# Performance work log

Hardware: AMD Instinct MI355X
Metric: run time of the kernel (lower is better)

## Reference

```python
import jax, jax.numpy as jnp
import numpy as np
import math

B, T, E, D = 4, 2048, 1024, 4

def _tau_init(t):
    a = 0.1 ** (1.0 / max(t - 1, 1))
    tt = -math.log(max(a, 1e-10))
    return math.log(math.exp(tt) - 1 + 1e-10)

def causal_ema(b, tau_raw):
    # h_t = alpha * h_{t-1} + b_t with alpha = exp(-softplus(tau_raw));
    # exactly equal to the conv1d with kernel exp(-tau*j) in the original.
    alpha = jnp.exp(-jax.nn.softplus(tau_raw)).astype(b.dtype)
    def step(h, bt):
        h = alpha * h + bt
        return h, h
    h0 = jnp.zeros((b.shape[0], b.shape[2]), b.dtype)
    _, hs = jax.lax.scan(step, h0, jnp.swapaxes(b, 0, 1))  # scan over T
    return jnp.swapaxes(hs, 0, 1)

def setup_inputs():
    key = jax.random.key(0)
    ks = jax.random.split(key, 10)
    s = 0.02
    return {
        "x": jax.random.normal(ks[0], (B, T, E), jnp.float32),
        "tau_ctx": jnp.float32(_tau_init(max(T // 2, 4))),
        "tau_raws": jnp.array([_tau_init(max(T // 2 ** i, 2)) for i in range(D)], jnp.float32),
        "Wg": jax.random.normal(ks[1], (E, 2 * E), jnp.float32) * s,
        "bg": jnp.full((E,), -0.5, jnp.float32),
        "Wn1": jax.random.normal(ks[2], (E // 4, E), jnp.float32) * s,
        "bn1": jnp.zeros((E // 4,), jnp.float32),
        "Wn2": jax.random.normal(ks[3], (D, E // 4), jnp.float32) * s,
        "bn2": jnp.zeros((D,), jnp.float32),
        "blend": jax.random.normal(ks[4], (D, E), jnp.float32) * s,
        "Wsoma": jax.random.normal(ks[5], (E, E), jnp.float32) * s,
        "bsoma": jnp.zeros((E,), jnp.float32),
        "Wtemp": jax.random.normal(ks[6], (E, E), jnp.float32) * s,
        "btemp": jnp.zeros((E,), jnp.float32),
        "Wout": jax.random.normal(ks[7], (E, E), jnp.float32) * s,
        "gamma": jnp.ones((E,), jnp.float32),
        "beta": jnp.zeros((E,), jnp.float32),
    }

def reference(x, tau_ctx, tau_raws, Wg, bg, Wn1, bn1, Wn2, bn2, blend, Wsoma, bsoma, Wtemp, btemp, Wout, gamma, beta):
    ctx = causal_ema(x, tau_ctx)                                   # (B,T,E)
    gate_in = jnp.concatenate([x, ctx], axis=-1)                   # (B,T,2E)
    wg = jax.nn.sigmoid(jnp.einsum('btc,ec->bte', gate_in, Wg) + bg)
    gated = x * wg
    h1 = jax.nn.gelu(jnp.einsum('btc,hc->bth', x, Wn1) + bn1, approximate=False)
    mod = 0.5 + jax.nn.sigmoid(jnp.einsum('bth,dh->btd', h1, Wn2) + bn2)  # (B,T,D)
    # neuromod_ema: modulate input then fixed-alpha EMA, one per dendrite
    traces = jax.vmap(lambda tau, m: causal_ema(gated * m[..., None], tau))(
        tau_raws, jnp.moveaxis(mod, -1, 0))                        # (D,B,T,E)
    blend_w = jax.nn.softmax(blend, axis=0)                        # (D,E)
    temporal = jnp.einsum('dbtc,dc->btc', traces, blend_w)
    gate = jax.nn.sigmoid(jnp.einsum('btc,ec->bte', temporal, Wtemp) + btemp)
    soma = jax.nn.gelu(jnp.einsum('btc,ec->bte', x, Wsoma) + bsoma, approximate=False)
    out = jnp.einsum('btc,ec->bte', soma * gate, Wout)
    mu = out.mean(-1, keepdims=True)
    var = out.var(-1, keepdims=True)
    return (out - mu) / jnp.sqrt(var + 1e-5) * gamma + beta
```

## Files before the change

### kernel.cpp

```cpp
#include <hip/hip_runtime.h>
#include <math.h>

#define B_DIM 4
#define T_DIM 2048
#define E_DIM 1024
#define M_ROWS (B_DIM*T_DIM)
#define NC 32
#define CL (T_DIM/NC)

typedef short short8 __attribute__((ext_vector_type(8)));
typedef float f32x4 __attribute__((ext_vector_type(4)));

__device__ __forceinline__ float bf2f(unsigned short u){
  union { unsigned int i; float f; } c; c.i = ((unsigned int)u) << 16; return c.f;
}
__device__ __forceinline__ unsigned short f2bf(float f){
  union { float f; unsigned int i; } c; c.f = f;
  unsigned int u = c.i;
  return (unsigned short)((u + 0x7FFFu + ((u >> 16) & 1u)) >> 16);
}
__device__ __forceinline__ unsigned int pack2(float a, float b){
  return (unsigned int)f2bf(a) | ((unsigned int)f2bf(b) << 16);
}
__device__ __forceinline__ float sigf(float x){ return 1.f/(1.f+__expf(-x)); }
__device__ __forceinline__ float geluf(float x){ return 0.5f*x*(1.f+erff(x*0.70710678118f)); }

__device__ __forceinline__ void glds16(const unsigned short* g, unsigned short* l){
  __builtin_amdgcn_global_load_lds((const __attribute__((address_space(1))) void*)g,
                                   (__attribute__((address_space(3))) void*)l, 16, 0, 0);
}

__device__ __forceinline__ void cvt4(const float* __restrict__ s, unsigned short* __restrict__ d){
  float4 v = *(const float4*)s;
  uint2 p; p.x = pack2(v.x, v.y); p.y = pack2(v.z, v.w);
  *(uint2*)d = p;
}

__global__ __launch_bounds__(256) void conv_all_k(
    const float* __restrict__ Wg, const float* __restrict__ Wsoma,
    const float* __restrict__ Wn1, const float* __restrict__ Wtemp,
    const float* __restrict__ Wout, const float* __restrict__ bsoma,
    const float* __restrict__ bn1,
    unsigned short* __restrict__ wg_bf, unsigned short* __restrict__ wsn1,
    unsigned short* __restrict__ wtemp_bf, unsigned short* __restrict__ wout_bf,
    float* __restrict__ bsn1){
  int u = blockIdx.x*256 + threadIdx.x;
  if (u < 524288){ cvt4(Wg + (size_t)u*4, wg_bf + (size_t)u*4); }
  else if (u < 786432){ u -= 524288; cvt4(Wsoma + (size_t)u*4, wsn1 + (size_t)u*4); }
  else if (u < 851968){ u -= 786432; cvt4(Wn1 + (size_t)u*4, wsn1 + 1048576 + (size_t)u*4); }
  else if (u < 1114112){ u -= 851968; cvt4(Wtemp + (size_t)u*4, wtemp_bf + (size_t)u*4); }
  else if (u < 1376256){ u -= 1114112; cvt4(Wout + (size_t)u*4, wout_bf + (size_t)u*4); }
  else if (u < 1376576){
    u -= 1376256; int i = u*4;
    float4 v = (i < 1024) ? *(const float4*)&bsoma[i] : *(const float4*)&bn1[i-1024];
    *(float4*)&bsn1[i] = v;
  }
}

__global__ __launch_bounds__(256) void ctx_carry_k(const float* __restrict__ x,
                                                   const float* __restrict__ tau_ctx,
                                                   float* __restrict__ car){
  int gid = blockIdx.x*256 + threadIdx.x;
  int e2 = (gid & 511)*2, bc = gid >> 9;
  int b = bc >> 5, chunk = bc & 31;
  float alpha = 1.f/(1.f+expf(tau_ctx[0]));
  const float2* xp = (const float2*)(x + ((size_t)b*T_DIM + chunk*CL)*E_DIM + e2);
  float h0 = 0.f, h1 = 0.f;
  #pragma unroll 8
  for (int t = 0; t < CL; t++){
    float2 v = xp[(size_t)t*512];
    h0 = alpha*h0 + v.x; h1 = alpha*h1 + v.y;
  }
  *(float2*)&car[(size_t)bc*E_DIM + e2] = make_float2(h0, h1);
}

__global__ __launch_bounds__(256) void ctx_scan_k(const float* __restrict__ x,
                                                  const float* __restrict__ tau_ctx,
                                                  const float* __restrict__ car,
                                                  unsigned short* __restrict__ gatein){
  int gid = blockIdx.x*256 + threadIdx.x;
  int e2 = (gid & 511)*2, bc = gid >> 9;
  int b = bc >> 5, chunk = bc & 31;
  float alpha = 1.f/(1.f+expf(tau_ctx[0]));
  float alphaL = powf(alpha, (float)CL);
  float h0 = 0.f, h1 = 0.f;
  for (int j = 0; j < chunk; j++){
    float2 c = *(const float2*)&car[(size_t)(b*NC + j)*E_DIM + e2];
    h0 = alphaL*h0 + c.x; h1 = alphaL*h1 + c.y;
  }
  const float2* xp = (const float2*)(x + ((size_t)b*T_DIM + chunk*CL)*E_DIM + e2);
  unsigned int* op = (unsigned int*)(gatein + ((size_t)(b*T_DIM + chunk*CL))*2048 + e2);
  #pragma unroll 4
  for (int t = 0; t < CL; t++){
    float2 v = xp[(size_t)t*512];
    h0 = alpha*h0 + v.x; h1 = alpha*h1 + v.y;
    op[(size_t)t*1024]       = pack2(v.x, v.y);
    op[(size_t)t*1024 + 512] = pack2(h0, h1);
  }
}

__global__ __launch_bounds__(256) void dend_carry_k(const unsigned short* __restrict__ gated,
                                                    const float* __restrict__ mod,
                                                    const float* __restrict__ tau_raws,
                                                    float* __restrict__ car){
  int gid = blockIdx.x*256 + threadIdx.x;
  int e2 = (gid & 511)*2, bc = gid >> 9;
  int b = bc >> 5, chunk = bc & 31;
  float a[4];
  #pragma unroll
  for (int d = 0; d < 4; d++) a[d] = 1.f/(1.f+expf(tau_raws[d]));
  const ushort2* gp = (const ushort2*)(gated + ((size_t)(b*T_DIM + chunk*CL))*E_DIM + e2);
  const float4* mp = (const float4*)(mod + (size_t)(b*T_DIM + chunk*CL)*4);
  float hx[4] = {0,0,0,0}, hy[4] = {0,0,0,0};
  #pragma unroll 4
  for (int t = 0; t < CL; t++){
    ushort2 gv = gp[(size_t)t*512];
    float gx = bf2f(gv.x), gy = bf2f(gv.y);
    float4 m4 = mp[t];
    hx[0] = a[0]*hx[0] + gx*m4.x; hy[0] = a[0]*hy[0] + gy*m4.x;
    hx[1] = a[1]*hx[1] + gx*m4.y; hy[1] = a[1]*hy[1] + gy*m4.y;
    hx[2] = a[2]*hx[2] + gx*m4.z; hy[2] = a[2]*hy[2] + gy*m4.z;
    hx[3] = a[3]*hx[3] + gx*m4.w; hy[3] = a[3]*hy[3] + gy*m4.w;
  }
  #pragma unroll
  for (int d = 0; d < 4; d++)
    *(float2*)&car[(size_t)d*131072 + (size_t)bc*E_DIM + e2] = make_float2(hx[d], hy[d]);
}

__global__ __launch_bounds__(256) void dend_scan_k(const unsigned short* __restrict__ gated,
                                                   const float* __restrict__ mod,
                                                   const float* __restrict__ tau_raws,
                                                   const float* __restrict__ car,
                                                   const float* __restrict__ blend,
                                                   unsigned short* __restrict__ temporal){
  int gid = blockIdx.x*256 + threadIdx.x;
  int e2 = (gid & 511)*2, bc = gid >> 9;
  int b = bc >> 5, chunk = bc & 31;
  float a[4], hx[4], hy[4];
  #pragma unroll
  for (int d = 0; d < 4; d++) a[d] = 1.f/(1.f+expf(tau_raws[d]));
  #pragma unroll
  for (int d = 0; d < 4; d++){
    float aL = powf(a[d], (float)CL);
    float h0 = 0.f, h1 = 0.f;
    for (int j = 0; j < chunk; j++){
      float2 c = *(const float2*)&car[(size_t)d*131072 + (size_t)(b*NC + j)*E_DIM + e2];
      h0 = aL*h0 + c.x; h1 = aL*h1 + c.y;
    }
    hx[d] = h0; hy[d] = h1;
  }
  float blx[4], bly[4];
  #pragma unroll
  for (int d = 0; d < 4; d++){
    float2 bl = *(const float2*)&blend[(size_t)d*E_DIM + e2];
    blx[d] = bl.x; bly[d] = bl.y;
  }
  float mxx = fmaxf(fmaxf(blx[0],blx[1]), fmaxf(blx[2],blx[3]));
  float mxy = fmaxf(fmaxf(bly[0],bly[1]), fmaxf(bly[2],bly[3]));
  float wx[4], wy[4], sx = 0.f, sy = 0.f;
  #pragma unroll
  for (int d = 0; d < 4; d++){ wx[d] = __expf(blx[d]-mxx); sx += wx[d];
                               wy[d] = __expf(bly[d]-mxy); sy += wy[d]; }
  float ix = 1.f/sx, iy = 1.f/sy;
  #pragma unroll
  for (int d = 0; d < 4; d++){ wx[d] *= ix; wy[d] *= iy; }

  const ushort2* gp = (const ushort2*)(gated + ((size_t)(b*T_DIM + chunk*CL))*E_DIM + e2);
  const float4* mp = (const float4*)(mod + (size_t)(b*T_DIM + chunk*CL)*4);
  unsigned int* op = (unsigned int*)(temporal + ((size_t)(b*T_DIM + chunk*CL))*E_DIM + e2);
  #pragma unroll 4
  for (int t = 0; t < CL; t++){
    ushort2 gv = gp[(size_t)t*512];
    float gx = bf2f(gv.x), gy = bf2f(gv.y);
    float4 m4 = mp[t];
    hx[0] = a[0]*hx[0] + gx*m4.x; hy[0] = a[0]*hy[0] + gy*m4.x;
    hx[1] = a[1]*hx[1] + gx*m4.y; hy[1] = a[1]*hy[1] + gy*m4.y;
    hx[2] = a[2]*hx[2] + gx*m4.z; hy[2] = a[2]*hy[2] + gy*m4.z;
    hx[3] = a[3]*hx[3] + gx*m4.w; hy[3] = a[3]*hy[3] + gy*m4.w;
    float tvx = wx[0]*hx[0] + wx[1]*hx[1] + wx[2]*hx[2] + wx[3]*hx[3];
    float tvy = wy[0]*hy[0] + wy[1]*hy[1] + wy[2]*hy[2] + wy[3]*hy[3];
    op[(size_t)t*512] = pack2(tvx, tvy);
  }
}

__global__ __launch_bounds__(256) void mod_k(const unsigned short* __restrict__ h1,
                                             const float* __restrict__ Wn2,
                                             const float* __restrict__ bn2,
                                             float* __restrict__ mod){
  int wave = threadIdx.x >> 6, lane = threadIdx.x & 63;
  int m = blockIdx.x*4 + wave;
  float p0=0.f,p1=0.f,p2=0.f,p3=0.f;
  for (int c = lane; c < 256; c += 64){
    float h = bf2f(h1[(size_t)m*256 + c]);
    p0 += h*Wn2[0*256 + c]; p1 += h*Wn2[1*256 + c];
    p2 += h*Wn2[2*256 + c]; p3 += h*Wn2[3*256 + c];
  }
  #pragma unroll
  for (int off = 32; off > 0; off >>= 1){
    p0 += __shfl_down(p0, off); p1 += __shfl_down(p1, off);
    p2 += __shfl_down(p2, off); p3 += __shfl_down(p3, off);
  }
  if (lane == 0){
    mod[(size_t)m*4 + 0] = 0.5f + sigf(p0 + bn2[0]);
    mod[(size_t)m*4 + 1] = 0.5f + sigf(p1 + bn2[1]);
    mod[(size_t)m*4 + 2] = 0.5f + sigf(p2 + bn2[2]);
    mod[(size_t)m*4 + 3] = 0.5f + sigf(p3 + bn2[3]);
  }
}

__global__ __launch_bounds__(256, 2) void gemm1_k(
    const unsigned short* __restrict__ gatein,
    const unsigned short* __restrict__ wg_bf,
    const unsigned short* __restrict__ wsn1,
    const float* __restrict__ bg,
    const float* __restrict__ bsn1,
    unsigned short* __restrict__ gated,
    unsigned short* __restrict__ soma,
    unsigned short* __restrict__ h1)
{
  __shared__ unsigned short sA[2][4096];
  __shared__ unsigned short sB[2][4096];
  const int tid = threadIdx.x;
  const int wv = tid >> 6, lane = tid & 63;
  const int quad = lane >> 4, l15 = lane & 15;
  const int wm = (wv & 1) * 64, wn = (wv >> 1) * 64;
  const int row0 = blockIdx.x * 128;
  const int by = blockIdx.y;

  int mode, colw0, K;
  const unsigned short* Bw;
  const float* bias;
  if (by < 8)       { mode = 0; colw0 = by*128;            Bw = wg_bf + (size_t)colw0*2048; K = 2048; bias = bg   + colw0; }
  else if (by < 16) { mode = 1; colw0 = (by-8)*128;        Bw = wsn1  + (size_t)colw0*1024; K = 1024; bias = bsn1 + colw0; }
  else              { mode = 2; colw0 = 1024 + (by-16)*128; Bw = wsn1 + (size_t)colw0*1024; K = 1024; bias = bsn1 + colw0; }

  const int r = tid >> 2, kc = (tid & 3) * 8;
  const unsigned short* pa0 = gatein + (size_t)(row0 + r)*2048      + kc;
  const unsigned short* pa1 = gatein + (size_t)(row0 + 64 + r)*2048 + kc;
  const unsigned short* pb0 = Bw + (size_t)r*K        + kc;
  const unsigned short* pb1 = Bw + (size_t)(64 + r)*K + kc;

  f32x4 acc[4][4];
  #pragma unroll
  for (int i = 0; i < 4; i++)
    #pragma unroll
    for (int j = 0; j < 4; j++) acc[i][j] = (f32x4){0.f,0.f,0.f,0.f};

  glds16(pa0, &sA[0][wv*512]);
  glds16(pa1, &sA[0][2048 + wv*512]);
  glds16(pb0, &sB[0][wv*512]);
  glds16(pb1, &sB[0][2048 + wv*512]);

  const int nk = K >> 5;
  for (int it = 0; it < nk; it++){
    __syncthreads();
    const int cur = it & 1, nxt = cur ^ 1;
    if (it + 1 < nk){
      const int ko = (it + 1) << 5;
      glds16(pa0 + ko, &sA[nxt][wv*512]);
      glds16(pa1 + ko, &sA[nxt][2048 + wv*512]);
      glds16(pb0 + ko, &sB[nxt][wv*512]);
      glds16(pb1 + ko, &sB[nxt][2048 + wv*512]);
    }
    short8 afr[4], bfr[4];
    #pragma unroll
    for (int i = 0; i < 4; i++) afr[i] = *(const short8*)&sA[cur][(wm + i*16 + l15)*32 + quad*8];
    #pragma unroll
    for (int j = 0; j < 4; j++) bfr[j] = *(const short8*)&sB[cur][(wn + j*16 + l15)*32 + quad*8];
    #pragma unroll
    for (int i = 0; i < 4; i++)
      #pragma unroll
      for (int j = 0; j < 4; j++)
        acc[i][j] = __builtin_amdgcn_mfma_f32_16x16x32_bf16(afr[i], bfr[j], acc[i][j], 0, 0, 0);
  }

  if (mode == 0){
    #pragma unroll
    for (int i = 0; i < 4; i++)
      #pragma unroll
      for (int j = 0; j < 4; j++){
        const int lc = wn + j*16 + l15;
        const int col = colw0 + lc;
        #pragma unroll
        for (int rr = 0; rr < 4; rr++){
          const int row = row0 + wm + i*16 + quad*4 + rr;
          float v = acc[i][j][rr] + bias[lc];
          float xv = bf2f(gatein[(size_t)row*2048 + col]);
          gated[(size_t)row*1024 + col] = f2bf(xv * sigf(v));
        }
      }
  } else if (mode == 1){
    #pragma unroll
    for (int i = 0; i < 4; i++)
      #pragma unroll
      for (int j = 0; j < 4; j++){
        const int lc = wn + j*16 + l15;
        const int col = colw0 + lc;
        #pragma unroll
        for (int rr = 0; rr < 4; rr++){
          const int row = row0 + wm + i*16 + quad*4 + rr;
          float v = acc[i][j][rr] + bias[lc];
          soma[(size_t)row*1024 + col] = f2bf(geluf(v));
        }
      }
  } else {
    #pragma unroll
    for (int i = 0; i < 4; i++)
      #pragma unroll
      for (int j = 0; j < 4; j++){
        const int lc = wn + j*16 + l15;
        const int col = colw0 - 1024 + lc;
        #pragma unroll
        for (int rr = 0; rr < 4; rr++){
          const int row = row0 + wm + i*16 + quad*4 + rr;
          float v = acc[i][j][rr] + bias[lc];
          h1[(size_t)row*256 + col] = f2bf(geluf(v));
        }
      }
  }
}

template<int EPI>
__global__ __launch_bounds__(256, 2) void gemm_k(
    const unsigned short* __restrict__ A,
    const unsigned short* __restrict__ Bw,
    const float* __restrict__ bias,
    const unsigned short* __restrict__ ebf,
    void* __restrict__ outp)
{
  __shared__ unsigned short sA[2][4096];
  __shared__ unsigned short sB[2][4096];
  const int tid = threadIdx.x;
  const int wv = tid >> 6, lane = tid & 63;
  const int quad = lane >> 4, l15 = lane & 15;
  const int wm = (wv & 1) * 64, wn = (wv >> 1) * 64;
  const int row0 = blockIdx.x * 128, col0 = blockIdx.y * 128;

  const int r = tid >> 2, kc = (tid & 3) * 8;
  const unsigned short* pa0 = A  + (size_t)(row0 + r)*1024      + kc;
  const unsigned short* pa1 = A  + (size_t)(row0 + 64 + r)*1024 + kc;
  const unsigned short* pb0 = Bw + (size_t)(col0 + r)*1024      + kc;
  const unsigned short* pb1 = Bw + (size_t)(col0 + 64 + r)*1024 + kc;

  f32x4 acc[4][4];
  #pragma unroll
  for (int i = 0; i < 4; i++)
    #pragma unroll
    for (int j = 0; j < 4; j++) acc[i][j] = (f32x4){0.f,0.f,0.f,0.f};

  glds16(pa0, &sA[0][wv*512]);
  glds16(pa1, &sA[0][2048 + wv*512]);
  glds16(pb0, &sB[0][wv*512]);
  glds16(pb1, &sB[0][2048 + wv*512]);

  for (int it = 0; it < 32; it++){
    __syncthreads();
    const int cur = it & 1, nxt = cur ^ 1;
    if (it + 1 < 32){
      const int ko = (it + 1) << 5;
      glds16(pa0 + ko, &sA[nxt][wv*512]);
      glds16(pa1 + ko, &sA[nxt][2048 + wv*512]);
      glds16(pb0 + ko, &sB[nxt][wv*512]);
      glds16(pb1 + ko, &sB[nxt][2048 + wv*512]);
    }
    short8 afr[4], bfr[4];
    #pragma unroll
    for (int i = 0; i < 4; i++) afr[i] = *(const short8*)&sA[cur][(wm + i*16 + l15)*32 + quad*8];
    #pragma unroll
    for (int j = 0; j < 4; j++) bfr[j] = *(const short8*)&sB[cur][(wn + j*16 + l15)*32 + quad*8];
    #pragma unroll
    for (int i = 0; i < 4; i++)
      #pragma unroll
      for (int j = 0; j < 4; j++)
        acc[i][j] = __builtin_amdgcn_mfma_f32_16x16x32_bf16(afr[i], bfr[j], acc[i][j], 0, 0, 0);
  }

  #pragma unroll
  for (int i = 0; i < 4; i++)
    #pragma unroll
    for (int j = 0; j < 4; j++){
      const int col = col0 + wn + j*16 + l15;
      #pragma unroll
      for (int rr = 0; rr < 4; rr++){
        const int row = row0 + wm + i*16 + quad*4 + rr;
        float v = acc[i][j][rr];
        size_t o = (size_t)row*1024 + col;
        if (EPI == 2){
          v += bias[col];
          ((unsigned short*)outp)[o] = f2bf(sigf(v) * bf2f(ebf[o]));
        } else {
          ((float*)outp)[o] = v;
        }
      }
    }
}

__global__ __launch_bounds__(256) void ln_k(const float* __restrict__ in,
                                            const float* __restrict__ gamma,
                                            const float* __restrict__ beta,
                                            float* __restrict__ out){
  __shared__ float s1[4], s2[4];
  int row = blockIdx.x, tid = threadIdx.x;
  float4 v = *(const float4*)&in[(size_t)row*1024 + tid*4];
  float s = v.x+v.y+v.z+v.w;
  float q = v.x*v.x+v.y*v.y+v.z*v.z+v.w*v.w;
  #pragma unroll
  for (int off = 32; off > 0; off >>= 1){ s += __shfl_down(s, off); q += __shfl_down(q, off); }
  int wave = tid >> 6, lane = tid & 63;
  if (lane == 0){ s1[wave] = s; s2[wave] = q; }
  __syncthreads();
  s = s1[0]+s1[1]+s1[2]+s1[3];
  q = s2[0]+s2[1]+s2[2]+s2[3];
  float mu = s*(1.f/1024.f);
  float var = q*(1.f/1024.f) - mu*mu;
  float rs = rsqrtf(var + 1e-5f);
  int c = tid*4;
  float4 g = *(const float4*)&gamma[c];
  float4 bb = *(const float4*)&beta[c];
  float4 o;
  o.x = (v.x-mu)*rs*g.x + bb.x;
  o.y = (v.y-mu)*rs*g.y + bb.y;
  o.z = (v.z-mu)*rs*g.z + bb.z;
  o.w = (v.w-mu)*rs*g.w + bb.w;
  *(float4*)&out[(size_t)row*1024 + c] = o;
}

extern "C" void kernel_launch(void* const* d_in, const int* in_sizes, int n_in,
                              void* d_out, int out_size, void* d_ws, size_t ws_size,
                              hipStream_t stream) {
  const float* x        = (const float*)d_in[0];
  const float* tau_ctx  = (const float*)d_in[1];
  const float* tau_raws = (const float*)d_in[2];
  const float* Wg       = (const float*)d_in[3];
  const float* bg       = (const float*)d_in[4];
  const float* Wn1      = (const float*)d_in[5];
  const float* bn1      = (const float*)d_in[6];
  const float* Wn2      = (const float*)d_in[7];
  const float* bn2      = (const float*)d_in[8];
  const float* blend    = (const float*)d_in[9];
  const float* Wsoma    = (const float*)d_in[10];
  const float* bsoma    = (const float*)d_in[11];
  const float* Wtemp    = (const float*)d_in[12];
  const float* btemp    = (const float*)d_in[13];
  const float* Wout     = (const float*)d_in[14];
  const float* gamma    = (const float*)d_in[15];
  const float* beta     = (const float*)d_in[16];

  char* ws = (char*)d_ws;
  unsigned short* gatein   = (unsigned short*)(ws + 0);
  float*          out_pre  = (float*)(ws + 0);
  unsigned short* wg_bf    = (unsigned short*)(ws + 33554432);
  unsigned short* wsn1     = (unsigned short*)(ws + 37748736);
  unsigned short* wtemp_bf = (unsigned short*)(ws + 40370176);
  unsigned short* wout_bf  = (unsigned short*)(ws + 42467328);
  float*          bsn1     = (float*)(ws + 44564480);
  unsigned short* h1_bf    = (unsigned short*)(ws + 44572672);
  float*          car_d    = (float*)(ws + 44572672);
  float*          car_ctx  = (float*)(ws + 48766976);
  float*          modbuf   = (float*)(ws + 48766976);
  unsigned short* gated    = (unsigned short*)(ws + 49291264);
  unsigned short* sg       = gated;
  unsigned short* temporal = (unsigned short*)(ws + 66068480);
  unsigned short* soma     = (unsigned short*)(ws + 82845696);

  conv_all_k<<<dim3(5378), dim3(256), 0, stream>>>(Wg, Wsoma, Wn1, Wtemp, Wout, bsoma, bn1,
                                                   wg_bf, wsn1, wtemp_bf, wout_bf, bsn1);

  ctx_carry_k<<<dim3(256), dim3(256), 0, stream>>>(x, tau_ctx, car_ctx);
  ctx_scan_k <<<dim3(256), dim3(256), 0, stream>>>(x, tau_ctx, car_ctx, gatein);

  gemm1_k<<<dim3(64, 18), dim3(256), 0, stream>>>(gatein, wg_bf, wsn1, bg, bsn1,
                                                  gated, soma, h1_bf);

  mod_k<<<dim3(M_ROWS/4), dim3(256), 0, stream>>>(h1_bf, Wn2, bn2, modbuf);

  dend_carry_k<<<dim3(256), dim3(256), 0, stream>>>(gated, modbuf, tau_raws, car_d);
  dend_scan_k <<<dim3(256), dim3(256), 0, stream>>>(gated, modbuf, tau_raws, car_d, blend, temporal);

  gemm_k<2><<<dim3(64, 8), dim3(256), 0, stream>>>(temporal, wtemp_bf, btemp, soma, sg);

  gemm_k<3><<<dim3(64, 8), dim3(256), 0, stream>>>(sg, wout_bf, nullptr, nullptr, out_pre);

  ln_k<<<dim3(M_ROWS), dim3(256), 0, stream>>>(out_pre, gamma, beta, (float*)d_out);
}
```

Baseline: 342.8 us.

## Fuse weight conversion with ctx carry, shrink GEMM tiles, one-wave-per-row LayerNorm

The weight-conversion kernel and the ctx carry kernel are merged into a single launch. The K=2048 gate GEMM in gemm1 is split into 64-row tiles, giving 26 column groups instead of 18. gemm_k now uses 64x128 tiles, doubling its grid. LayerNorm handles one row per wave with xor shuffles, which removes the LDS reduction and the block barrier. The aim is better CU occupancy and load balance on the 256-CU GPU and less launch overhead, at the cost of more B-tile reloads per output.

After: 358.1 us. 4.5% more time.

```diff
diff --git a/kernel.cpp b/kernel.cpp
--- a/kernel.cpp
+++ b/kernel.cpp
@@ -36,42 +36,42 @@
   *(uint2*)d = p;
 }
 
-__global__ __launch_bounds__(256) void conv_all_k(
+__global__ __launch_bounds__(256) void conv_carry_k(
     const float* __restrict__ Wg, const float* __restrict__ Wsoma,
     const float* __restrict__ Wn1, const float* __restrict__ Wtemp,
     const float* __restrict__ Wout, const float* __restrict__ bsoma,
     const float* __restrict__ bn1,
     unsigned short* __restrict__ wg_bf, unsigned short* __restrict__ wsn1,
     unsigned short* __restrict__ wtemp_bf, unsigned short* __restrict__ wout_bf,
-    float* __restrict__ bsn1){
-  int u = blockIdx.x*256 + threadIdx.x;
-  if (u < 524288){ cvt4(Wg + (size_t)u*4, wg_bf + (size_t)u*4); }
-  else if (u < 786432){ u -= 524288; cvt4(Wsoma + (size_t)u*4, wsn1 + (size_t)u*4); }
-  else if (u < 851968){ u -= 786432; cvt4(Wn1 + (size_t)u*4, wsn1 + 1048576 + (size_t)u*4); }
-  else if (u < 1114112){ u -= 851968; cvt4(Wtemp + (size_t)u*4, wtemp_bf + (size_t)u*4); }
-  else if (u < 1376256){ u -= 1114112; cvt4(Wout + (size_t)u*4, wout_bf + (size_t)u*4); }
-  else if (u < 1376576){
-    u -= 1376256; int i = u*4;
-    float4 v = (i < 1024) ? *(const float4*)&bsoma[i] : *(const float4*)&bn1[i-1024];
-    *(float4*)&bsn1[i] = v;
-  }
-}
-
-__global__ __launch_bounds__(256) void ctx_carry_k(const float* __restrict__ x,
-                                                   const float* __restrict__ tau_ctx,
-                                                   float* __restrict__ car){
-  int gid = blockIdx.x*256 + threadIdx.x;
-  int e2 = (gid & 511)*2, bc = gid >> 9;
-  int b = bc >> 5, chunk = bc & 31;
-  float alpha = 1.f/(1.f+expf(tau_ctx[0]));
-  const float2* xp = (const float2*)(x + ((size_t)b*T_DIM + chunk*CL)*E_DIM + e2);
-  float h0 = 0.f, h1 = 0.f;
-  #pragma unroll 8
-  for (int t = 0; t < CL; t++){
-    float2 v = xp[(size_t)t*512];
-    h0 = alpha*h0 + v.x; h1 = alpha*h1 + v.y;
-  }
-  *(float2*)&car[(size_t)bc*E_DIM + e2] = make_float2(h0, h1);
+    float* __restrict__ bsn1,
+    const float* __restrict__ x, const float* __restrict__ tau_ctx,
+    float* __restrict__ car){
+  if (blockIdx.x < 5378){
+    int u = blockIdx.x*256 + threadIdx.x;
+    if (u < 524288){ cvt4(Wg + (size_t)u*4, wg_bf + (size_t)u*4); }
+    else if (u < 786432){ u -= 524288; cvt4(Wsoma + (size_t)u*4, wsn1 + (size_t)u*4); }
+    else if (u < 851968){ u -= 786432; cvt4(Wn1 + (size_t)u*4, wsn1 + 1048576 + (size_t)u*4); }
+    else if (u < 1114112){ u -= 851968; cvt4(Wtemp + (size_t)u*4, wtemp_bf + (size_t)u*4); }
+    else if (u < 1376256){ u -= 1114112; cvt4(Wout + (size_t)u*4, wout_bf + (size_t)u*4); }
+    else if (u < 1376576){
+      u -= 1376256; int i = u*4;
+      float4 v = (i < 1024) ? *(const float4*)&bsoma[i] : *(const float4*)&bn1[i-1024];
+      *(float4*)&bsn1[i] = v;
+    }
+  } else {
+    int gid = (blockIdx.x - 5378)*256 + threadIdx.x;
+    int e2 = (gid & 511)*2, bc = gid >> 9;
+    int b = bc >> 5, chunk = bc & 31;
+    float alpha = 1.f/(1.f+expf(tau_ctx[0]));
+    const float2* xp = (const float2*)(x + ((size_t)b*T_DIM + chunk*CL)*E_DIM + e2);
+    float h0 = 0.f, h1 = 0.f;
+    #pragma unroll 8
+    for (int t = 0; t < CL; t++){
+      float2 v = xp[(size_t)t*512];
+      h0 = alpha*h0 + v.x; h1 = alpha*h1 + v.y;
+    }
+    *(float2*)&car[(size_t)bc*E_DIM + e2] = make_float2(h0, h1);
+  }
 }
 
 __global__ __launch_bounds__(256) void ctx_scan_k(const float* __restrict__ x,
@@ -223,60 +223,51 @@
   const int tid = threadIdx.x;
   const int wv = tid >> 6, lane = tid & 63;
   const int quad = lane >> 4, l15 = lane & 15;
-  const int wm = (wv & 1) * 64, wn = (wv >> 1) * 64;
-  const int row0 = blockIdx.x * 128;
   const int by = blockIdx.y;
-
-  int mode, colw0, K;
-  const unsigned short* Bw;
-  const float* bias;
-  if (by < 8)       { mode = 0; colw0 = by*128;            Bw = wg_bf + (size_t)colw0*2048; K = 2048; bias = bg   + colw0; }
-  else if (by < 16) { mode = 1; colw0 = (by-8)*128;        Bw = wsn1  + (size_t)colw0*1024; K = 1024; bias = bsn1 + colw0; }
-  else              { mode = 2; colw0 = 1024 + (by-16)*128; Bw = wsn1 + (size_t)colw0*1024; K = 1024; bias = bsn1 + colw0; }
-
   const int r = tid >> 2, kc = (tid & 3) * 8;
-  const unsigned short* pa0 = gatein + (size_t)(row0 + r)*2048      + kc;
-  const unsigned short* pa1 = gatein + (size_t)(row0 + 64 + r)*2048 + kc;
-  const unsigned short* pb0 = Bw + (size_t)r*K        + kc;
-  const unsigned short* pb1 = Bw + (size_t)(64 + r)*K + kc;
-
-  f32x4 acc[4][4];
-  #pragma unroll
-  for (int i = 0; i < 4; i++)
-    #pragma unroll
-    for (int j = 0; j < 4; j++) acc[i][j] = (f32x4){0.f,0.f,0.f,0.f};
-
-  glds16(pa0, &sA[0][wv*512]);
-  glds16(pa1, &sA[0][2048 + wv*512]);
-  glds16(pb0, &sB[0][wv*512]);
-  glds16(pb1, &sB[0][2048 + wv*512]);
-
-  const int nk = K >> 5;
-  for (int it = 0; it < nk; it++){
-    __syncthreads();
-    const int cur = it & 1, nxt = cur ^ 1;
-    if (it + 1 < nk){
-      const int ko = (it + 1) << 5;
-      glds16(pa0 + ko, &sA[nxt][wv*512]);
-      glds16(pa1 + ko, &sA[nxt][2048 + wv*512]);
-      glds16(pb0 + ko, &sB[nxt][wv*512]);
-      glds16(pb1 + ko, &sB[nxt][2048 + wv*512]);
-    }
-    short8 afr[4], bfr[4];
-    #pragma unroll
-    for (int i = 0; i < 4; i++) afr[i] = *(const short8*)&sA[cur][(wm + i*16 + l15)*32 + quad*8];
-    #pragma unroll
-    for (int j = 0; j < 4; j++) bfr[j] = *(const short8*)&sB[cur][(wn + j*16 + l15)*32 + quad*8];
-    #pragma unroll
-    for (int i = 0; i < 4; i++)
-      #pragma unroll
-      for (int j = 0; j < 4; j++)
-        acc[i][j] = __builtin_amdgcn_mfma_f32_16x16x32_bf16(afr[i], bfr[j], acc[i][j], 0, 0, 0);
-  }
-
-  if (mode == 0){
-    #pragma unroll
-    for (int i = 0; i < 4; i++)
+
+  if (by < 16){
+    const int colw0 = (by & 7) * 128;
+    const int row0 = blockIdx.x * 128 + ((by >> 3) ? 64 : 0);
+    const unsigned short* Bw = wg_bf + (size_t)colw0 * 2048;
+    const unsigned short* pa0 = gatein + (size_t)(row0 + r)*2048 + kc;
+    const unsigned short* pb0 = Bw + (size_t)r*2048        + kc;
+    const unsigned short* pb1 = Bw + (size_t)(64 + r)*2048 + kc;
+    const int wm = (wv & 1) * 32, wn = (wv >> 1) * 64;
+
+    f32x4 acc[2][4];
+    #pragma unroll
+    for (int i = 0; i < 2; i++)
+      #pragma unroll
+      for (int j = 0; j < 4; j++) acc[i][j] = (f32x4){0.f,0.f,0.f,0.f};
+
+    glds16(pa0, &sA[0][wv*512]);
+    glds16(pb0, &sB[0][wv*512]);
+    glds16(pb1, &sB[0][2048 + wv*512]);
+
+    for (int it = 0; it < 64; it++){
+      __syncthreads();
+      const int cur = it & 1, nxt = cur ^ 1;
+      if (it + 1 < 64){
+        const int ko = (it + 1) << 5;
+        glds16(pa0 + ko, &sA[nxt][wv*512]);
+        glds16(pb0 + ko, &sB[nxt][wv*512]);
+        glds16(pb1 + ko, &sB[nxt][2048 + wv*512]);
+      }
+      short8 afr[2], bfr[4];
+      #pragma unroll
+      for (int i = 0; i < 2; i++) afr[i] = *(const short8*)&sA[cur][(wm + i*16 + l15)*32 + quad*8];
+      #pragma unroll
+      for (int j = 0; j < 4; j++) bfr[j] = *(const short8*)&sB[cur][(wn + j*16 + l15)*32 + quad*8];
+      #pragma unroll
+      for (int i = 0; i < 2; i++)
+        #pragma unroll
+        for (int j = 0; j < 4; j++)
+          acc[i][j] = __builtin_amdgcn_mfma_f32_16x16x32_bf16(afr[i], bfr[j], acc[i][j], 0, 0, 0);
+    }
+
+    #pragma unroll
+    for (int i = 0; i < 2; i++)
       #pragma unroll
       for (int j = 0; j < 4; j++){
         const int lc = wn + j*16 + l15;
@@ -284,37 +275,68 @@
         #pragma unroll
         for (int rr = 0; rr < 4; rr++){
           const int row = row0 + wm + i*16 + quad*4 + rr;
-          float v = acc[i][j][rr] + bias[lc];
+          float v = acc[i][j][rr] + bg[col];
           float xv = bf2f(gatein[(size_t)row*2048 + col]);
           gated[(size_t)row*1024 + col] = f2bf(xv * sigf(v));
         }
       }
-  } else if (mode == 1){
+  } else {
+    const int ish1 = (by >= 24);
+    const int colw0 = ish1 ? (by - 24)*128 : (by - 16)*128;
+    const int row0 = blockIdx.x * 128;
+    const unsigned short* Bw = wsn1 + (size_t)(ish1 ? 1024 + colw0 : colw0) * 1024;
+    const float* bias = bsn1 + (ish1 ? 1024 + colw0 : colw0);
+    const unsigned short* pa0 = gatein + (size_t)(row0 + r)*2048      + kc;
+    const unsigned short* pa1 = gatein + (size_t)(row0 + 64 + r)*2048 + kc;
+    const unsigned short* pb0 = Bw + (size_t)r*1024        + kc;
+    const unsigned short* pb1 = Bw + (size_t)(64 + r)*1024 + kc;
+    const int wm = (wv & 1) * 64, wn = (wv >> 1) * 64;
+
+    f32x4 acc[4][4];
+    #pragma unroll
+    for (int i = 0; i < 4; i++)
+      #pragma unroll
+      for (int j = 0; j < 4; j++) acc[i][j] = (f32x4){0.f,0.f,0.f,0.f};
+
+    glds16(pa0, &sA[0][wv*512]);
+    glds16(pa1, &sA[0][2048 + wv*512]);
+    glds16(pb0, &sB[0][wv*512]);
+    glds16(pb1, &sB[0][2048 + wv*512]);
+
+    for (int it = 0; it < 32; it++){
+      __syncthreads();
+      const int cur = it & 1, nxt = cur ^ 1;
+      if (it + 1 < 32){
+        const int ko = (it + 1) << 5;
+        glds16(pa0 + ko, &sA[nxt][wv*512]);
+        glds16(pa1 + ko, &sA[nxt][2048 + wv*512]);
+        glds16(pb0 + ko, &sB[nxt][wv*512]);
+        glds16(pb1 + ko, &sB[nxt][2048 + wv*512]);
+      }
+      short8 afr[4], bfr[4];
+      #pragma unroll
+      for (int i = 0; i < 4; i++) afr[i] = *(const short8*)&sA[cur][(wm + i*16 + l15)*32 + quad*8];
+      #pragma unroll
+      for (int j = 0; j < 4; j++) bfr[j] = *(const short8*)&sB[cur][(wn + j*16 + l15)*32 + quad*8];
+      #pragma unroll
+      for (int i = 0; i < 4; i++)
+        #pragma unroll
+        for (int j = 0; j < 4; j++)
+          acc[i][j] = __builtin_amdgcn_mfma_f32_16x16x32_bf16(afr[i], bfr[j], acc[i][j], 0, 0, 0);
+    }
+
     #pragma unroll
     for (int i = 0; i < 4; i++)
       #pragma unroll
       for (int j = 0; j < 4; j++){
         const int lc = wn + j*16 + l15;
-        const int col = colw0 + lc;
         #pragma unroll
         for (int rr = 0; rr < 4; rr++){
           const int row = row0 + wm + i*16 + quad*4 + rr;
           float v = acc[i][j][rr] + bias[lc];
-          soma[(size_t)row*1024 + col] = f2bf(geluf(v));
-        }
-      }
-  } else {
-    #pragma unroll
-    for (int i = 0; i < 4; i++)
-      #pragma unroll
-      for (int j = 0; j < 4; j++){
-        const int lc = wn + j*16 + l15;
-        const int col = colw0 - 1024 + lc;
-        #pragma unroll
-        for (int rr = 0; rr < 4; rr++){
-          const int row = row0 + wm + i*16 + quad*4 + rr;
-          float v = acc[i][j][rr] + bias[lc];
-          h1[(size_t)row*256 + col] = f2bf(geluf(v));
+          float g = geluf(v);
+          if (ish1) h1[(size_t)row*256 + colw0 + lc] = f2bf(g);
+          else      soma[(size_t)row*1024 + colw0 + lc] = f2bf(g);
         }
       }
   }
@@ -328,28 +350,26 @@
     const unsigned short* __restrict__ ebf,
     void* __restrict__ outp)
 {
-  __shared__ unsigned short sA[2][4096];
+  __shared__ unsigned short sA[2][2048];
   __shared__ unsigned short sB[2][4096];
   const int tid = threadIdx.x;
   const int wv = tid >> 6, lane = tid & 63;
   const int quad = lane >> 4, l15 = lane & 15;
-  const int wm = (wv & 1) * 64, wn = (wv >> 1) * 64;
-  const int row0 = blockIdx.x * 128, col0 = blockIdx.y * 128;
+  const int wm = (wv & 1) * 32, wn = (wv >> 1) * 64;
+  const int row0 = blockIdx.x * 64, col0 = blockIdx.y * 128;
 
   const int r = tid >> 2, kc = (tid & 3) * 8;
   const unsigned short* pa0 = A  + (size_t)(row0 + r)*1024      + kc;
-  const unsigned short* pa1 = A  + (size_t)(row0 + 64 + r)*1024 + kc;
   const unsigned short* pb0 = Bw + (size_t)(col0 + r)*1024      + kc;
   const unsigned short* pb1 = Bw + (size_t)(col0 + 64 + r)*1024 + kc;
 
-  f32x4 acc[4][4];
-  #pragma unroll
-  for (int i = 0; i < 4; i++)
+  f32x4 acc[2][4];
+  #pragma unroll
+  for (int i = 0; i < 2; i++)
     #pragma unroll
     for (int j = 0; j < 4; j++) acc[i][j] = (f32x4){0.f,0.f,0.f,0.f};
 
   glds16(pa0, &sA[0][wv*512]);
-  glds16(pa1, &sA[0][2048 + wv*512]);
   glds16(pb0, &sB[0][wv*512]);
   glds16(pb1, &sB[0][2048 + wv*512]);
 
@@ -359,24 +379,23 @@
     if (it + 1 < 32){
       const int ko = (it + 1) << 5;
       glds16(pa0 + ko, &sA[nxt][wv*512]);
-      glds16(pa1 + ko, &sA[nxt][2048 + wv*512]);
       glds16(pb0 + ko, &sB[nxt][wv*512]);
       glds16(pb1 + ko, &sB[nxt][2048 + wv*512]);
     }
-    short8 afr[4], bfr[4];
-    #pragma unroll
-    for (int i = 0; i < 4; i++) afr[i] = *(const short8*)&sA[cur][(wm + i*16 + l15)*32 + quad*8];
+    short8 afr[2], bfr[4];
+    #pragma unroll
+    for (int i = 0; i < 2; i++) afr[i] = *(const short8*)&sA[cur][(wm + i*16 + l15)*32 + quad*8];
     #pragma unroll
     for (int j = 0; j < 4; j++) bfr[j] = *(const short8*)&sB[cur][(wn + j*16 + l15)*32 + quad*8];
     #pragma unroll
-    for (int i = 0; i < 4; i++)
+    for (int i = 0; i < 2; i++)
       #pragma unroll
       for (int j = 0; j < 4; j++)
         acc[i][j] = __builtin_amdgcn_mfma_f32_16x16x32_bf16(afr[i], bfr[j], acc[i][j], 0, 0, 0);
   }
 
   #pragma unroll
-  for (int i = 0; i < 4; i++)
+  for (int i = 0; i < 2; i++)
     #pragma unroll
     for (int j = 0; j < 4; j++){
       const int col = col0 + wn + j*16 + l15;
@@ -399,30 +418,38 @@
                                             const float* __restrict__ gamma,
                                             const float* __restrict__ beta,
                                             float* __restrict__ out){
-  __shared__ float s1[4], s2[4];
-  int row = blockIdx.x, tid = threadIdx.x;
-  float4 v = *(const float4*)&in[(size_t)row*1024 + tid*4];
-  float s = v.x+v.y+v.z+v.w;
-  float q = v.x*v.x+v.y*v.y+v.z*v.z+v.w*v.w;
-  #pragma unroll
-  for (int off = 32; off > 0; off >>= 1){ s += __shfl_down(s, off); q += __shfl_down(q, off); }
-  int wave = tid >> 6, lane = tid & 63;
-  if (lane == 0){ s1[wave] = s; s2[wave] = q; }
-  __syncthreads();
-  s = s1[0]+s1[1]+s1[2]+s1[3];
-  q = s2[0]+s2[1]+s2[2]+s2[3];
+  int wv = threadIdx.x >> 6, lane = threadIdx.x & 63;
+  int row = blockIdx.x*4 + wv;
+  const float4* ip = (const float4*)&in[(size_t)row*1024];
+  float4 v[4];
+  float s = 0.f, q = 0.f;
+  #pragma unroll
+  for (int k = 0; k < 4; k++){
+    v[k] = ip[lane + 64*k];
+    s += v[k].x + v[k].y + v[k].z + v[k].w;
+    q += v[k].x*v[k].x + v[k].y*v[k].y + v[k].z*v[k].z + v[k].w*v[k].w;
+  }
+  #pragma unroll
+  for (int off = 32; off > 0; off >>= 1){
+    s += __shfl_xor(s, off); q += __shfl_xor(q, off);
+  }
   float mu = s*(1.f/1024.f);
   float var = q*(1.f/1024.f) - mu*mu;
   float rs = rsqrtf(var + 1e-5f);
-  int c = tid*4;
-  float4 g = *(const float4*)&gamma[c];
-  float4 bb = *(const float4*)&beta[c];
-  float4 o;
-  o.x = (v.x-mu)*rs*g.x + bb.x;
-  o.y = (v.y-mu)*rs*g.y + bb.y;
-  o.z = (v.z-mu)*rs*g.z + bb.z;
-  o.w = (v.w-mu)*rs*g.w + bb.w;
-  *(float4*)&out[(size_t)row*1024 + c] = o;
+  const float4* gp = (const float4*)gamma;
+  const float4* bp = (const float4*)beta;
+  float4* op = (float4*)&out[(size_t)row*1024];
+  #pragma unroll
+  for (int k = 0; k < 4; k++){
+    int idx = lane + 64*k;
+    float4 g = gp[idx], bb = bp[idx];
+    float4 o;
+    o.x = (v[k].x-mu)*rs*g.x + bb.x;
+    o.y = (v[k].y-mu)*rs*g.y + bb.y;
+    o.z = (v[k].z-mu)*rs*g.z + bb.z;
+    o.w = (v[k].w-mu)*rs*g.w + bb.w;
+    op[idx] = o;
+  }
 }
 
 extern "C" void kernel_launch(void* const* d_in, const int* in_sizes, int n_in,
@@ -463,13 +490,13 @@
   unsigned short* temporal = (unsigned short*)(ws + 66068480);
   unsigned short* soma     = (unsigned short*)(ws + 82845696);
 
-  conv_all_k<<<dim3(5378), dim3(256), 0, stream>>>(Wg, Wsoma, Wn1, Wtemp, Wout, bsoma, bn1,
-                                                   wg_bf, wsn1, wtemp_bf, wout_bf, bsn1);
-
-  ctx_carry_k<<<dim3(256), dim3(256), 0, stream>>>(x, tau_ctx, car_ctx);
-  ctx_scan_k <<<dim3(256), dim3(256), 0, stream>>>(x, tau_ctx, car_ctx, gatein);
-
-  gemm1_k<<<dim3(64, 18), dim3(256), 0, stream>>>(gatein, wg_bf, wsn1, bg, bsn1,
+  conv_carry_k<<<dim3(5634), dim3(256), 0, stream>>>(Wg, Wsoma, Wn1, Wtemp, Wout, bsoma, bn1,
+                                                     wg_bf, wsn1, wtemp_bf, wout_bf, bsn1,
+                                                     x, tau_ctx, car_ctx);
+
+  ctx_scan_k<<<dim3(256), dim3(256), 0, stream>>>(x, tau_ctx, car_ctx, gatein);
+
+  gemm1_k<<<dim3(64, 26), dim3(256), 0, stream>>>(gatein, wg_bf, wsn1, bg, bsn1,
                                                   gated, soma, h1_bf);
 
   mod_k<<<dim3(M_ROWS/4), dim3(256), 0, stream>>>(h1_bf, Wn2, bn2, modbuf);
@@ -477,9 +504,9 @@
   dend_carry_k<<<dim3(256), dim3(256), 0, stream>>>(gated, modbuf, tau_raws, car_d);
   dend_scan_k <<<dim3(256), dim3(256), 0, stream>>>(gated, modbuf, tau_raws, car_d, blend, temporal);
 
-  gemm_k<2><<<dim3(64, 8), dim3(256), 0, stream>>>(temporal, wtemp_bf, btemp, soma, sg);
-
-  gemm_k<3><<<dim3(64, 8), dim3(256), 0, stream>>>(sg, wout_bf, nullptr, nullptr, out_pre);
-
-  ln_k<<<dim3(M_ROWS), dim3(256), 0, stream>>>(out_pre, gamma, beta, (float*)d_out);
-}
+  gemm_k<2><<<dim3(128, 8), dim3(256), 0, stream>>>(temporal, wtemp_bf, btemp, soma, sg);
+
+  gemm_k<3><<<dim3(128, 8), dim3(256), 0, stream>>>(sg, wout_bf, nullptr, nullptr, out_pre);
+
+  ln_k<<<dim3(M_ROWS/4), dim3(256), 0, stream>>>(out_pre, gamma, beta, (float*)d_out);
+}
```

## Fuse weight conversion with ctx carry, relayout GEMM LDS tiles, per-wave layernorm

Applied to the files above, without the earlier changes.

Merges the weight-conversion kernel and the context-carry kernel into one launch, dispatching on block index, to save a launch and let the two independent jobs overlap. Both GEMM kernels change their global-to-LDS load mapping so that each wave loads one k-slice of 8 elements for 64 rows. The LDS tile becomes k-group-major, which changes the fragment read addresses and is meant to reduce bank conflicts. Layernorm now uses one wave per row with shuffle-xor reductions and no shared memory or block barrier.

Measured after the change: 421.8 us. 23.0% more time.

```diff
diff --git a/kernel.cpp b/kernel.cpp
--- a/kernel.cpp
+++ b/kernel.cpp
@@ -36,42 +36,42 @@
   *(uint2*)d = p;
 }
 
-__global__ __launch_bounds__(256) void conv_all_k(
+__global__ __launch_bounds__(256) void conv_carry_k(
     const float* __restrict__ Wg, const float* __restrict__ Wsoma,
     const float* __restrict__ Wn1, const float* __restrict__ Wtemp,
     const float* __restrict__ Wout, const float* __restrict__ bsoma,
     const float* __restrict__ bn1,
     unsigned short* __restrict__ wg_bf, unsigned short* __restrict__ wsn1,
     unsigned short* __restrict__ wtemp_bf, unsigned short* __restrict__ wout_bf,
-    float* __restrict__ bsn1){
-  int u = blockIdx.x*256 + threadIdx.x;
-  if (u < 524288){ cvt4(Wg + (size_t)u*4, wg_bf + (size_t)u*4); }
-  else if (u < 786432){ u -= 524288; cvt4(Wsoma + (size_t)u*4, wsn1 + (size_t)u*4); }
-  else if (u < 851968){ u -= 786432; cvt4(Wn1 + (size_t)u*4, wsn1 + 1048576 + (size_t)u*4); }
-  else if (u < 1114112){ u -= 851968; cvt4(Wtemp + (size_t)u*4, wtemp_bf + (size_t)u*4); }
-  else if (u < 1376256){ u -= 1114112; cvt4(Wout + (size_t)u*4, wout_bf + (size_t)u*4); }
-  else if (u < 1376576){
-    u -= 1376256; int i = u*4;
-    float4 v = (i < 1024) ? *(const float4*)&bsoma[i] : *(const float4*)&bn1[i-1024];
-    *(float4*)&bsn1[i] = v;
-  }
-}
-
-__global__ __launch_bounds__(256) void ctx_carry_k(const float* __restrict__ x,
-                                                   const float* __restrict__ tau_ctx,
-                                                   float* __restrict__ car){
-  int gid = blockIdx.x*256 + threadIdx.x;
-  int e2 = (gid & 511)*2, bc = gid >> 9;
-  int b = bc >> 5, chunk = bc & 31;
-  float alpha = 1.f/(1.f+expf(tau_ctx[0]));
-  const float2* xp = (const float2*)(x + ((size_t)b*T_DIM + chunk*CL)*E_DIM + e2);
-  float h0 = 0.f, h1 = 0.f;
-  #pragma unroll 8
-  for (int t = 0; t < CL; t++){
-    float2 v = xp[(size_t)t*512];
-    h0 = alpha*h0 + v.x; h1 = alpha*h1 + v.y;
-  }
-  *(float2*)&car[(size_t)bc*E_DIM + e2] = make_float2(h0, h1);
+    float* __restrict__ bsn1,
+    const float* __restrict__ x, const float* __restrict__ tau_ctx,
+    float* __restrict__ car){
+  if (blockIdx.x < 5378){
+    int u = blockIdx.x*256 + threadIdx.x;
+    if (u < 524288){ cvt4(Wg + (size_t)u*4, wg_bf + (size_t)u*4); }
+    else if (u < 786432){ u -= 524288; cvt4(Wsoma + (size_t)u*4, wsn1 + (size_t)u*4); }
+    else if (u < 851968){ u -= 786432; cvt4(Wn1 + (size_t)u*4, wsn1 + 1048576 + (size_t)u*4); }
+    else if (u < 1114112){ u -= 851968; cvt4(Wtemp + (size_t)u*4, wtemp_bf + (size_t)u*4); }
+    else if (u < 1376256){ u -= 1114112; cvt4(Wout + (size_t)u*4, wout_bf + (size_t)u*4); }
+    else if (u < 1376576){
+      u -= 1376256; int i = u*4;
+      float4 v = (i < 1024) ? *(const float4*)&bsoma[i] : *(const float4*)&bn1[i-1024];
+      *(float4*)&bsn1[i] = v;
+    }
+  } else {
+    int gid = (blockIdx.x - 5378)*256 + threadIdx.x;
+    int e2 = (gid & 511)*2, bc = gid >> 9;
+    int b = bc >> 5, chunk = bc & 31;
+    float alpha = 1.f/(1.f+expf(tau_ctx[0]));
+    const float2* xp = (const float2*)(x + ((size_t)b*T_DIM + chunk*CL)*E_DIM + e2);
+    float h0 = 0.f, h1 = 0.f;
+    #pragma unroll 8
+    for (int t = 0; t < CL; t++){
+      float2 v = xp[(size_t)t*512];
+      h0 = alpha*h0 + v.x; h1 = alpha*h1 + v.y;
+    }
+    *(float2*)&car[(size_t)bc*E_DIM + e2] = make_float2(h0, h1);
+  }
 }
 
 __global__ __launch_bounds__(256) void ctx_scan_k(const float* __restrict__ x,
@@ -230,15 +230,14 @@
   int mode, colw0, K;
   const unsigned short* Bw;
   const float* bias;
-  if (by < 8)       { mode = 0; colw0 = by*128;            Bw = wg_bf + (size_t)colw0*2048; K = 2048; bias = bg   + colw0; }
-  else if (by < 16) { mode = 1; colw0 = (by-8)*128;        Bw = wsn1  + (size_t)colw0*1024; K = 1024; bias = bsn1 + colw0; }
-  else              { mode = 2; colw0 = 1024 + (by-16)*128; Bw = wsn1 + (size_t)colw0*1024; K = 1024; bias = bsn1 + colw0; }
-
-  const int r = tid >> 2, kc = (tid & 3) * 8;
-  const unsigned short* pa0 = gatein + (size_t)(row0 + r)*2048      + kc;
-  const unsigned short* pa1 = gatein + (size_t)(row0 + 64 + r)*2048 + kc;
-  const unsigned short* pb0 = Bw + (size_t)r*K        + kc;
-  const unsigned short* pb1 = Bw + (size_t)(64 + r)*K + kc;
+  if (by < 8)       { mode = 0; colw0 = by*128;             Bw = wg_bf + (size_t)colw0*2048; K = 2048; bias = bg   + colw0; }
+  else if (by < 16) { mode = 1; colw0 = (by-8)*128;         Bw = wsn1  + (size_t)colw0*1024; K = 1024; bias = bsn1 + colw0; }
+  else              { mode = 2; colw0 = 1024 + (by-16)*128; Bw = wsn1  + (size_t)colw0*1024; K = 1024; bias = bsn1 + colw0; }
+
+  const unsigned short* pa0 = gatein + (size_t)(row0 + lane)*2048 + wv*8;
+  const unsigned short* pa1 = pa0 + (size_t)64*2048;
+  const unsigned short* pb0 = Bw + (size_t)lane*K + wv*8;
+  const unsigned short* pb1 = pb0 + (size_t)64*K;
 
   f32x4 acc[4][4];
   #pragma unroll
@@ -246,10 +245,10 @@
     #pragma unroll
     for (int j = 0; j < 4; j++) acc[i][j] = (f32x4){0.f,0.f,0.f,0.f};
 
-  glds16(pa0, &sA[0][wv*512]);
-  glds16(pa1, &sA[0][2048 + wv*512]);
-  glds16(pb0, &sB[0][wv*512]);
-  glds16(pb1, &sB[0][2048 + wv*512]);
+  glds16(pa0, &sA[0][wv*1024]);
+  glds16(pa1, &sA[0][wv*1024 + 512]);
+  glds16(pb0, &sB[0][wv*1024]);
+  glds16(pb1, &sB[0][wv*1024 + 512]);
 
   const int nk = K >> 5;
   for (int it = 0; it < nk; it++){
@@ -257,16 +256,16 @@
     const int cur = it & 1, nxt = cur ^ 1;
     if (it + 1 < nk){
       const int ko = (it + 1) << 5;
-      glds16(pa0 + ko, &sA[nxt][wv*512]);
-      glds16(pa1 + ko, &sA[nxt][2048 + wv*512]);
-      glds16(pb0 + ko, &sB[nxt][wv*512]);
-      glds16(pb1 + ko, &sB[nxt][2048 + wv*512]);
+      glds16(pa0 + ko, &sA[nxt][wv*1024]);
+      glds16(pa1 + ko, &sA[nxt][wv*1024 + 512]);
+      glds16(pb0 + ko, &sB[nxt][wv*1024]);
+      glds16(pb1 + ko, &sB[nxt][wv*1024 + 512]);
     }
     short8 afr[4], bfr[4];
     #pragma unroll
-    for (int i = 0; i < 4; i++) afr[i] = *(const short8*)&sA[cur][(wm + i*16 + l15)*32 + quad*8];
-    #pragma unroll
-    for (int j = 0; j < 4; j++) bfr[j] = *(const short8*)&sB[cur][(wn + j*16 + l15)*32 + quad*8];
+    for (int i = 0; i < 4; i++) afr[i] = *(const short8*)&sA[cur][(quad*128 + wm + i*16 + l15)*8];
+    #pragma unroll
+    for (int j = 0; j < 4; j++) bfr[j] = *(const short8*)&sB[cur][(quad*128 + wn + j*16 + l15)*8];
     #pragma unroll
     for (int i = 0; i < 4; i++)
       #pragma unroll
@@ -336,11 +335,10 @@
   const int wm = (wv & 1) * 64, wn = (wv >> 1) * 64;
   const int row0 = blockIdx.x * 128, col0 = blockIdx.y * 128;
 
-  const int r = tid >> 2, kc = (tid & 3) * 8;
-  const unsigned short* pa0 = A  + (size_t)(row0 + r)*1024      + kc;
-  const unsigned short* pa1 = A  + (size_t)(row0 + 64 + r)*1024 + kc;
-  const unsigned short* pb0 = Bw + (size_t)(col0 + r)*1024      + kc;
-  const unsigned short* pb1 = Bw + (size_t)(col0 + 64 + r)*1024 + kc;
+  const unsigned short* pa0 = A  + (size_t)(row0 + lane)*1024 + wv*8;
+  const unsigned short* pa1 = pa0 + (size_t)64*1024;
+  const unsigned short* pb0 = Bw + (size_t)(col0 + lane)*1024 + wv*8;
+  const unsigned short* pb1 = pb0 + (size_t)64*1024;
 
   f32x4 acc[4][4];
   #pragma unroll
@@ -348,26 +346,26 @@
     #pragma unroll
     for (int j = 0; j < 4; j++) acc[i][j] = (f32x4){0.f,0.f,0.f,0.f};
 
-  glds16(pa0, &sA[0][wv*512]);
-  glds16(pa1, &sA[0][2048 + wv*512]);
-  glds16(pb0, &sB[0][wv*512]);
-  glds16(pb1, &sB[0][2048 + wv*512]);
+  glds16(pa0, &sA[0][wv*1024]);
+  glds16(pa1, &sA[0][wv*1024 + 512]);
+  glds16(pb0, &sB[0][wv*1024]);
+  glds16(pb1, &sB[0][wv*1024 + 512]);
 
   for (int it = 0; it < 32; it++){
     __syncthreads();
     const int cur = it & 1, nxt = cur ^ 1;
     if (it + 1 < 32){
       const int ko = (it + 1) << 5;
-      glds16(pa0 + ko, &sA[nxt][wv*512]);
-      glds16(pa1 + ko, &sA[nxt][2048 + wv*512]);
-      glds16(pb0 + ko, &sB[nxt][wv*512]);
-      glds16(pb1 + ko, &sB[nxt][2048 + wv*512]);
+      glds16(pa0 + ko, &sA[nxt][wv*1024]);
+      glds16(pa1 + ko, &sA[nxt][wv*1024 + 512]);
+      glds16(pb0 + ko, &sB[nxt][wv*1024]);
+      glds16(pb1 + ko, &sB[nxt][wv*1024 + 512]);
     }
     short8 afr[4], bfr[4];
     #pragma unroll
-    for (int i = 0; i < 4; i++) afr[i] = *(const short8*)&sA[cur][(wm + i*16 + l15)*32 + quad*8];
-    #pragma unroll
-    for (int j = 0; j < 4; j++) bfr[j] = *(const short8*)&sB[cur][(wn + j*16 + l15)*32 + quad*8];
+    for (int i = 0; i < 4; i++) afr[i] = *(const short8*)&sA[cur][(quad*128 + wm + i*16 + l15)*8];
+    #pragma unroll
+    for (int j = 0; j < 4; j++) bfr[j] = *(const short8*)&sB[cur][(quad*128 + wn + j*16 + l15)*8];
     #pragma unroll
     for (int i = 0; i < 4; i++)
       #pragma unroll
@@ -399,30 +397,38 @@
                                             const float* __restrict__ gamma,
                                             const float* __restrict__ beta,
                                             float* __restrict__ out){
-  __shared__ float s1[4], s2[4];
-  int row = blockIdx.x, tid = threadIdx.x;
-  float4 v = *(const float4*)&in[(size_t)row*1024 + tid*4];
-  float s = v.x+v.y+v.z+v.w;
-  float q = v.x*v.x+v.y*v.y+v.z*v.z+v.w*v.w;
-  #pragma unroll
-  for (int off = 32; off > 0; off >>= 1){ s += __shfl_down(s, off); q += __shfl_down(q, off); }
-  int wave = tid >> 6, lane = tid & 63;
-  if (lane == 0){ s1[wave] = s; s2[wave] = q; }
-  __syncthreads();
-  s = s1[0]+s1[1]+s1[2]+s1[3];
-  q = s2[0]+s2[1]+s2[2]+s2[3];
+  int wv = threadIdx.x >> 6, lane = threadIdx.x & 63;
+  int row = blockIdx.x*4 + wv;
+  const float4* ip = (const float4*)&in[(size_t)row*1024];
+  float4 v[4];
+  float s = 0.f, q = 0.f;
+  #pragma unroll
+  for (int k = 0; k < 4; k++){
+    v[k] = ip[lane + 64*k];
+    s += v[k].x + v[k].y + v[k].z + v[k].w;
+    q += v[k].x*v[k].x + v[k].y*v[k].y + v[k].z*v[k].z + v[k].w*v[k].w;
+  }
+  #pragma unroll
+  for (int off = 32; off > 0; off >>= 1){
+    s += __shfl_xor(s, off); q += __shfl_xor(q, off);
+  }
   float mu = s*(1.f/1024.f);
   float var = q*(1.f/1024.f) - mu*mu;
   float rs = rsqrtf(var + 1e-5f);
-  int c = tid*4;
-  float4 g = *(const float4*)&gamma[c];
-  float4 bb = *(const float4*)&beta[c];
-  float4 o;
-  o.x = (v.x-mu)*rs*g.x + bb.x;
-  o.y = (v.y-mu)*rs*g.y + bb.y;
-  o.z = (v.z-mu)*rs*g.z + bb.z;
-  o.w = (v.w-mu)*rs*g.w + bb.w;
-  *(float4*)&out[(size_t)row*1024 + c] = o;
+  const float4* gp = (const float4*)gamma;
+  const float4* bp = (const float4*)beta;
+  float4* op = (float4*)&out[(size_t)row*1024];
+  #pragma unroll
+  for (int k = 0; k < 4; k++){
+    int idx = lane + 64*k;
+    float4 g = gp[idx], bb = bp[idx];
+    float4 o;
+    o.x = (v[k].x-mu)*rs*g.x + bb.x;
+    o.y = (v[k].y-mu)*rs*g.y + bb.y;
+    o.z = (v[k].z-mu)*rs*g.z + bb.z;
+    o.w = (v[k].w-mu)*rs*g.w + bb.w;
+    op[idx] = o;
+  }
 }
 
 extern "C" void kernel_launch(void* const* d_in, const int* in_sizes, int n_in,
@@ -463,11 +469,11 @@
   unsigned short* temporal = (unsigned short*)(ws + 66068480);
   unsigned short* soma     = (unsigned short*)(ws + 82845696);
 
-  conv_all_k<<<dim3(5378), dim3(256), 0, stream>>>(Wg, Wsoma, Wn1, Wtemp, Wout, bsoma, bn1,
-                                                   wg_bf, wsn1, wtemp_bf, wout_bf, bsn1);
-
-  ctx_carry_k<<<dim3(256), dim3(256), 0, stream>>>(x, tau_ctx, car_ctx);
-  ctx_scan_k <<<dim3(256), dim3(256), 0, stream>>>(x, tau_ctx, car_ctx, gatein);
+  conv_carry_k<<<dim3(5634), dim3(256), 0, stream>>>(Wg, Wsoma, Wn1, Wtemp, Wout, bsoma, bn1,
+                                                     wg_bf, wsn1, wtemp_bf, wout_bf, bsn1,
+                                                     x, tau_ctx, car_ctx);
+
+  ctx_scan_k<<<dim3(256), dim3(256), 0, stream>>>(x, tau_ctx, car_ctx, gatein);
 
   gemm1_k<<<dim3(64, 18), dim3(256), 0, stream>>>(gatein, wg_bf, wsn1, bg, bsn1,
                                                   gated, soma, h1_bf);
@@ -481,5 +487,5 @@
 
   gemm_k<3><<<dim3(64, 8), dim3(256), 0, stream>>>(sg, wout_bf, nullptr, nullptr, out_pre);
 
-  ln_k<<<dim3(M_ROWS), dim3(256), 0, stream>>>(out_pre, gamma, beta, (float*)d_out);
-}
+  ln_k<<<dim3(M_ROWS/4), dim3(256), 0, stream>>>(out_pre, gamma, beta, (float*)d_out);
+}
```
